# Kernel tuning notes

Measured on AMD Instinct MI355X. Metric: run time of the kernel, lower is better.

The kernel has to match this reference:

```python
import jax, jax.numpy as jnp
import numpy as np
jax.config.update("jax_enable_x64", True)

MAX_DEPTH = 21
SENTINEL = np.int64(2 ** 62)  # pads invalid (consumed) slots; > any real morton code


def split_by3(n):
    n = n & 2097151
    n = (n | (n << 32)) & 8725724278095871
    n = (n | (n << 16)) & 8725728556220671
    n = (n | (n << 8)) & 1157144660301377551
    n = (n | (n << 4)) & 1207822528635744451
    n = (n | (n << 2)) & 1317624576693539401
    return n


def _unique_agg(codes, feats):
    # codes: [N] sorted int64 (SENTINEL-padded at the end); feats: [N, F]
    # Emulates torch.unique_consecutive + scatter_add with fixed shapes.
    N = codes.shape[0]
    is_new = jnp.concatenate([jnp.ones((1,), dtype=bool), codes[1:] != codes[:-1]])
    seg = jnp.cumsum(is_new) - 1  # consecutive-group id (reverse index)
    agg = jax.ops.segment_sum(feats, seg, num_segments=N)
    ucodes = jnp.full((N,), SENTINEL, dtype=jnp.int64).at[seg].set(codes)
    count = jnp.sum(is_new & (codes != SENTINEL)).astype(jnp.int32)
    return ucodes, agg, count


def setup_inputs() -> dict:
    key = jax.random.key(0)
    N = 262144
    new_cloud = jax.random.normal(key, (N, 4), dtype=jnp.float32)
    leaf_size = jnp.full((3,), 0.1, dtype=jnp.float32)
    return {"new_cloud": new_cloud, "leaf_size": leaf_size}


def reference(new_cloud, leaf_size):
    xyz = new_cloud[:, :3]
    n = new_cloud.shape[0]
    # aggregated features: [count=1, xyz, xyz^2, extra cols]
    feats = jnp.concatenate(
        [jnp.ones((n, 1), new_cloud.dtype), xyz, xyz * xyz, new_cloud[:, 3:]], axis=1
    )
    origin = jnp.min(xyz, axis=0) - 0.5 * leaf_size
    ijk = jnp.floor((xyz - origin) / leaf_size).astype(jnp.int64)
    s = split_by3(ijk)
    codes = s[:, 0] | (s[:, 1] << 1) | (s[:, 2] << 2)
    order = jnp.argsort(codes)
    codes = codes[order]
    feats = feats[order]
    mc, ag, cnt = _unique_agg(codes, feats)
    mcs, ags, cnts = [mc], [ag], [cnt]
    for d in range(1, MAX_DEPTH):
        shifted = jnp.where(mc == SENTINEL, SENTINEL, mc >> 3)
        mc, ag, cnt = _unique_agg(shifted, ag)
        mcs.append(mc)
        ags.append(ag)
        cnts.append(cnt)
    # [MAX_DEPTH, N] codes (SENTINEL-padded), [MAX_DEPTH, N, F] aggregates (zero-padded), [MAX_DEPTH] valid counts
    return jnp.stack(mcs), jnp.stack(ags), jnp.stack(cnts)
```

## Files before the change

kernel.cpp:

```cpp
#include <hip/hip_runtime.h>
#include <stdint.h>

static constexpr int L0N = 2097152;
static constexpr int O1 = 0,      S1 = 262144;
static constexpr int O2 = 262144, S2 = 32768;
static constexpr int O3 = 294912, S3 = 4096;
static constexpr int O4 = 299008, S4 = 512;
static constexpr int O5 = 300032, S5 = 64;
static constexpr int O6 = 301056, S6 = 8;
static constexpr int O7 = 302080;
static constexpr int UP_TOT = 303104;
static constexpr int UNBLK = 296;

__device__ __forceinline__ unsigned s3_r9(unsigned n){
  n &= 0x3FFu;
  n = (n | (n << 16)) & 0x030000FFu;
  n = (n | (n << 8))  & 0x0300F00Fu;
  n = (n | (n << 4))  & 0x030C30C3u;
  n = (n | (n << 2))  & 0x09249249u;
  return n;
}

__device__ __forceinline__ void wave_block_min3(float& mx, float& my, float& mz, int tid){
  #pragma unroll
  for (int o = 32; o; o >>= 1){
    mx = fminf(mx, __shfl_down(mx, o, 64));
    my = fminf(my, __shfl_down(my, o, 64));
    mz = fminf(mz, __shfl_down(mz, o, 64));
  }
  __shared__ float sm[3][4];
  int lane = tid & 63, wid = tid >> 6;
  if (lane == 0){ sm[0][wid] = mx; sm[1][wid] = my; sm[2][wid] = mz; }
  __syncthreads();
  if (tid == 0){
    for (int w = 1; w < 4; w++){
      mx = fminf(mx, sm[0][w]); my = fminf(my, sm[1][w]); mz = fminf(mz, sm[2][w]);
    }
  }
}

__global__ void kminzero_r9(const float4* __restrict__ cloud, int n,
                            int* __restrict__ C0, float* __restrict__ pmins){
  int gid = blockIdx.x * blockDim.x + threadIdx.x;
  int gstride = gridDim.x * blockDim.x;
  int4 z = {0,0,0,0};
  for (int v = gid; v < L0N / 4; v += gstride)
    ((int4*)C0)[v] = z;
  float mx = INFINITY, my = INFINITY, mz = INFINITY;
  for (int i = gid; i < n; i += gstride){
    float4 p = cloud[i];
    mx = fminf(mx, p.x); my = fminf(my, p.y); mz = fminf(mz, p.z);
  }
  wave_block_min3(mx, my, mz, threadIdx.x);
  if (threadIdx.x == 0){
    pmins[3 * blockIdx.x + 0] = mx;
    pmins[3 * blockIdx.x + 1] = my;
    pmins[3 * blockIdx.x + 2] = mz;
  }
}

__global__ void kmin2_r9(const float* __restrict__ pmins, float* __restrict__ mins){
  int t = threadIdx.x;
  float mx = pmins[3 * t + 0];
  float my = pmins[3 * t + 1];
  float mz = pmins[3 * t + 2];
  wave_block_min3(mx, my, mz, t);
  if (t == 0){ mins[0] = mx; mins[1] = my; mins[2] = mz; }
}

__global__ void kA_r9(const float4* __restrict__ cloud, const float* __restrict__ leaf,
                      const float* __restrict__ mins, int n,
                      int* __restrict__ C0, int2* __restrict__ CR){
  int i = blockIdx.x * blockDim.x + threadIdx.x;
  if (i >= n) return;
  float lx = leaf[0], ly = leaf[1], lz = leaf[2];
  float ox = mins[0] - 0.5f * lx;
  float oy = mins[1] - 0.5f * ly;
  float oz = mins[2] - 0.5f * lz;
  float4 p = cloud[i];
  int ix = (int)floorf((p.x - ox) / lx);
  int iy = (int)floorf((p.y - oy) / ly);
  int iz = (int)floorf((p.z - oz) / lz);
  ix = min(max(ix, 0), 127); iy = min(max(iy, 0), 127); iz = min(max(iz, 0), 127);
  int code = (int)(s3_r9((unsigned)ix) | (s3_r9((unsigned)iy) << 1) | (s3_r9((unsigned)iz) << 2));
  int rank = atomicAdd(C0 + code, 1);
  CR[i] = {code, rank};
}

__device__ __forceinline__ int block_scan_incl(int v, int tid, int* total){
  __shared__ int w4[4];
  __syncthreads();
  int lane = tid & 63, wid = tid >> 6;
  #pragma unroll
  for (int o = 1; o < 64; o <<= 1){
    int n = __shfl_up(v, o, 64);
    if (lane >= o) v += n;
  }
  if (lane == 63) w4[wid] = v;
  __syncthreads();
  if (tid < 4){
    int w = w4[tid];
    #pragma unroll
    for (int o = 1; o < 4; o <<= 1){
      int n = __shfl_up(w, o, 4);
      if (tid >= o) w += n;
    }
    w4[tid] = w;
  }
  __syncthreads();
  if (wid > 0) v += w4[wid - 1];
  *total = w4[3];
  return v;
}

__global__ void ksA1_r9(const int* __restrict__ C0, int* __restrict__ cntTot,
                        int* __restrict__ flagTot){
  int b = blockIdx.x, t = threadIdx.x;
  const int4* c4 = (const int4*)(C0 + (size_t)b * 2048 + t * 8);
  int4 a = c4[0], d = c4[1];
  int cs = a.x + a.y + a.z + a.w + d.x + d.y + d.z + d.w;
  int fs = (a.x!=0)+(a.y!=0)+(a.z!=0)+(a.w!=0)+(d.x!=0)+(d.y!=0)+(d.z!=0)+(d.w!=0);
  int ctot, ftot;
  block_scan_incl(cs, t, &ctot);
  block_scan_incl(fs, t, &ftot);
  if (t == 0){ cntTot[b] = ctot; flagTot[b] = ftot; }
}

__global__ void ksA2_r9(const int* __restrict__ cntTot, const int* __restrict__ flagTot,
                        int* __restrict__ cntBase, int* __restrict__ flagBase,
                        float* __restrict__ cnts){
  int t = threadIdx.x;
  int ccarry = 0, fcarry = 0;
  for (int c = 0; c < 1024; c += 256){
    int cv = cntTot[c + t], fv = flagTot[c + t];
    int ctot, ftot;
    int ci = block_scan_incl(cv, t, &ctot);
    int fi = block_scan_incl(fv, t, &ftot);
    cntBase[c + t] = ccarry + (ci - cv);
    flagBase[c + t] = fcarry + (fi - fv);
    ccarry += ctot; fcarry += ftot;
  }
  if (t == 0) cnts[0] = (float)fcarry;
}

__global__ void ksA3_r9(const int* __restrict__ C0, const int* __restrict__ cntBase,
                        int* __restrict__ E){
  int b = blockIdx.x, t = threadIdx.x;
  const int4* c4 = (const int4*)(C0 + (size_t)b * 2048 + t * 8);
  int4 a = c4[0], d = c4[1];
  int k[8] = {a.x, a.y, a.z, a.w, d.x, d.y, d.z, d.w};
  int cs = k[0]+k[1]+k[2]+k[3]+k[4]+k[5]+k[6]+k[7];
  int tot;
  int incl = block_scan_incl(cs, t, &tot);
  int e = cntBase[b] + (incl - cs);
  int ev[8];
  #pragma unroll
  for (int c = 0; c < 8; c++){ ev[c] = e; e += k[c]; }
  int4* e4 = (int4*)(E + (size_t)b * 2048 + t * 8);
  e4[0] = {ev[0], ev[1], ev[2], ev[3]};
  e4[1] = {ev[4], ev[5], ev[6], ev[7]};
}

__global__ void kplace_r9(const float4* __restrict__ cloud, const int2* __restrict__ CR,
                          const int* __restrict__ E, int n, float4* __restrict__ S){
  int i = blockIdx.x * blockDim.x + threadIdx.x;
  if (i >= n) return;
  int2 cr = CR[i];
  S[E[cr.x] + cr.y] = cloud[i];
}

__global__ void kbuild1f_r9(const float4* __restrict__ S, const int* __restrict__ C0,
                            const int* __restrict__ E, const int* __restrict__ flagBase,
                            float* __restrict__ PU, int* __restrict__ CU,
                            float* __restrict__ out, int N){
  int p = blockIdx.x * blockDim.x + threadIdx.x;
  int b = blockIdx.x;
  int s0 = 8 * p;
  const int4* c4 = (const int4*)(C0 + s0);
  int4 ca = c4[0], cb = c4[1];
  int k[8] = {ca.x, ca.y, ca.z, ca.w, cb.x, cb.y, cb.z, cb.w};
  const int4* e4 = (const int4*)(E + s0);
  int4 ea = e4[0], eb = e4[1];
  int eo[8] = {ea.x, ea.y, ea.z, ea.w, eb.x, eb.y, eb.z, eb.w};
  float4 recA[8], recB[8];
  float4 pa = {0,0,0,0}, pb = {0,0,0,0};
  int fs = 0;
  #pragma unroll
  for (int c = 0; c < 8; c++){
    if (k[c] > 0){
      float4 a = {0,0,0,0}, bb = {0,0,0,0};
      int base = eo[c];
      for (int j = 0; j < k[c]; j++){
        float4 pt = S[base + j];
        a.x += 1.0f;        a.y += pt.x;        a.z += pt.y;        a.w += pt.z;
        bb.x += pt.x*pt.x;  bb.y += pt.y*pt.y;  bb.z += pt.z*pt.z;  bb.w += pt.w;
      }
      recA[c] = a; recB[c] = bb;
      pa.x += a.x; pa.y += a.y; pa.z += a.z; pa.w += a.w;
      pb.x += bb.x; pb.y += bb.y; pb.z += bb.z; pb.w += bb.w;
      fs++;
    }
  }
  int tot;
  int incl = block_scan_incl(fs, threadIdx.x, &tot);
  int pos = flagBase[b] + (incl - fs);
  size_t MCS = (size_t)21 * N;
  #pragma unroll
  for (int c = 0; c < 8; c++){
    if (k[c] > 0){
      out[pos] = (float)(s0 + c);
      float4* ag = (float4*)(out + MCS + (size_t)pos * 8);
      ag[0] = recA[c]; ag[1] = recB[c];
      pos++;
    }
  }
  float4* prec = (float4*)(PU + (size_t)p * 8);
  prec[0] = pa; prec[1] = pb;
  CU[p] = (int)pa.x;
}

__device__ __forceinline__ void build_one_r9(float* __restrict__ PU, int* __restrict__ CU,
                                             int srcOff, int dstOff, int p){
  const float4* s = (const float4*)(PU + (size_t)(srcOff + 8 * p) * 8);
  float4 a = {0,0,0,0}, b = {0,0,0,0};
  #pragma unroll
  for (int c = 0; c < 8; c++){
    float4 u = s[2 * c], v = s[2 * c + 1];
    a.x += u.x; a.y += u.y; a.z += u.z; a.w += u.w;
    b.x += v.x; b.y += v.y; b.z += v.z; b.w += v.w;
  }
  float4* d = (float4*)(PU + (size_t)(dstOff + p) * 8);
  d[0] = a; d[1] = b;
  CU[dstOff + p] = (int)a.x;
}

__global__ void kbuild_r9(float* __restrict__ PU, int* __restrict__ CU,
                          int srcOff, int dstOff, int ndst){
  int p = blockIdx.x * blockDim.x + threadIdx.x;
  if (p >= ndst) return;
  build_one_r9(PU, CU, srcOff, dstOff, p);
}

__global__ void kbuildtail_r9(float* __restrict__ PU, int* __restrict__ CU){
  for (int i = O4 + S4 + threadIdx.x; i < UP_TOT; i += blockDim.x)
    CU[i] = 0;
  __syncthreads();
  const int so[4]   = {O3, O4, O5, O6};
  const int dofs[4] = {O4, O5, O6, O7};
  const int nd[4]   = {S4, S5, S6, 1};
  for (int l = 0; l < 4; l++){
    for (int p = threadIdx.x; p < nd[l]; p += blockDim.x)
      build_one_r9(PU, CU, so[l], dofs[l], p);
    __syncthreads();
  }
}

__global__ void kscan1_r9(const int* __restrict__ CU, int* __restrict__ partials){
  int b = blockIdx.x, t = threadIdx.x;
  int4 v = ((const int4*)CU)[(size_t)b * 256 + t];
  int c = (v.x != 0) + (v.y != 0) + (v.z != 0) + (v.w != 0);
  int tot;
  block_scan_incl(c, t, &tot);
  if (t == 0) partials[b] = tot;
}

__global__ void kscan2_r9(const int* __restrict__ partials, int* __restrict__ base,
                          float* __restrict__ cnts){
  int t = threadIdx.x;
  __shared__ int s[UNBLK];
  for (int i = t; i < UNBLK; i += 256) s[i] = partials[i];
  __syncthreads();
  const int bb[8] = {0, 256, 288, 292, 293, 294, 295, 296};
  for (int L = 0; L < 7; L++){
    int beg = bb[L], end = bb[L + 1];
    int carry = 0;
    for (int c = beg; c < end; c += 256){
      int idx = c + t;
      int v = (idx < end) ? s[idx] : 0;
      int tot;
      int incl = block_scan_incl(v, t, &tot);
      if (idx < end) base[idx] = carry + (incl - v);
      carry += tot;
    }
    if (t == 0){
      if (L < 6) cnts[L + 1] = (float)carry;
      else { for (int d = 7; d < 21; d++) cnts[d] = (float)carry; }
    }
  }
}

__global__ void kscan3_r9(const float* __restrict__ PU, const int* __restrict__ CU,
                          const int* __restrict__ base, float* __restrict__ out, int N){
  int b = blockIdx.x, t = threadIdx.x;
  int lvl, soff;
  if      (b < 256){ lvl = 1; soff = O1; }
  else if (b < 288){ lvl = 2; soff = O2; }
  else if (b < 292){ lvl = 3; soff = O3; }
  else if (b < 293){ lvl = 4; soff = O4; }
  else if (b < 294){ lvl = 5; soff = O5; }
  else if (b < 295){ lvl = 6; soff = O6; }
  else             { lvl = 7; soff = O7; }
  int slot0 = b * 1024 + t * 4;
  int4 v = ((const int4*)CU)[(size_t)b * 256 + t];
  int fl[4] = { v.x != 0, v.y != 0, v.z != 0, v.w != 0 };
  int c = fl[0] + fl[1] + fl[2] + fl[3];
  int tot;
  int incl = block_scan_incl(c, t, &tot);
  int p = base[b] + (incl - c);
  size_t MCS = (size_t)21 * N;
  #pragma unroll
  for (int kk = 0; kk < 4; kk++){
    if (fl[kk]){
      int slot = slot0 + kk;
      out[(size_t)lvl * N + p] = (float)(slot - soff);
      const float4* rec = (const float4*)(PU + (size_t)slot * 8);
      float4* ag = (float4*)(out + MCS + ((size_t)lvl * N + p) * 8);
      ag[0] = rec[0]; ag[1] = rec[1];
      p++;
    }
  }
}

__global__ void kfinal_r9(const float* __restrict__ PU, float* __restrict__ out, int N){
  size_t MCS = (size_t)21 * N;
  int i = threadIdx.x;
  if (i < 104){
    int d = 8 + (i >> 3), q = i & 7;
    out[MCS + ((size_t)d * N) * 8 + q] = PU[(size_t)O7 * 8 + q];
  } else if (i < 117){
    int d = 8 + (i - 104);
    out[(size_t)d * N] = 0.0f;
  }
}

extern "C" void kernel_launch(void* const* d_in, const int* in_sizes, int n_in,
                              void* d_out, int out_size, void* d_ws, size_t ws_size,
                              hipStream_t stream){
  int ci = 0, li = 1;
  if (n_in >= 2 && in_sizes[0] == 3){ ci = 1; li = 0; }
  const float4* cloud = (const float4*)d_in[ci];
  const float*  leaf  = (const float*)d_in[li];
  int N = in_sizes[ci] / 4;

  float* out = (float*)d_out;
  float* PU   = (float*)d_ws;
  int*   C0   = (int*)(PU + (size_t)UP_TOT * 8);
  int*   CU   = C0 + L0N;
  int*   E    = CU + UP_TOT;
  int2*  CR   = (int2*)(E + L0N);
  float4* S   = (float4*)(CR + N);
  int* cntTot = (int*)(S + N);
  int* flagTot = cntTot + 1024;
  int* cntBase = flagTot + 1024;
  int* flagBase = cntBase + 1024;
  int* partU  = flagBase + 1024;
  int* baseU  = partU + UNBLK;
  float* pmins = (float*)(baseU + UNBLK);
  float* mins  = pmins + 768;
  float* cnts  = out + (size_t)189 * N;

  kminzero_r9<<<256, 256, 0, stream>>>(cloud, N, C0, pmins);
  kmin2_r9<<<1, 256, 0, stream>>>(pmins, mins);

  kA_r9<<<(N + 255) / 256, 256, 0, stream>>>(cloud, leaf, mins, N, C0, CR);
  ksA1_r9<<<1024, 256, 0, stream>>>(C0, cntTot, flagTot);
  ksA2_r9<<<1,    256, 0, stream>>>(cntTot, flagTot, cntBase, flagBase, cnts);
  ksA3_r9<<<1024, 256, 0, stream>>>(C0, cntBase, E);
  kplace_r9<<<(N + 255) / 256, 256, 0, stream>>>(cloud, CR, E, N, S);

  kbuild1f_r9<<<1024, 256, 0, stream>>>(S, C0, E, flagBase, PU, CU, out, N);
  kbuild_r9<<<128, 256, 0, stream>>>(PU, CU, O1, O2, S2);
  kbuild_r9<<<16,  256, 0, stream>>>(PU, CU, O2, O3, S3);
  kbuildtail_r9<<<1, 256, 0, stream>>>(PU, CU);

  kscan1_r9<<<UNBLK, 256, 0, stream>>>(CU, partU);
  kscan2_r9<<<1,     256, 0, stream>>>(partU, baseU, cnts);
  kscan3_r9<<<UNBLK, 256, 0, stream>>>(PU, CU, baseU, out, N);
  kfinal_r9<<<1, 128, 0, stream>>>(PU, out, N);
}
```

Baseline: 304.6 us.

## Fuse pipeline into fewer launches with decoupled look-back scans and grid spin barriers

Reduces the kernel count from fifteen to six. The min-reduction finalize moves into the binning kernel through an atomic flag. The three-pass count/flag scans become single-pass decoupled look-back scans. Place and level-1 build are merged behind a grid-wide spin barrier, as are the upper-level builds. The aim is to remove launch gaps and tiny serial kernels. The cost is that the spin barriers assume all blocks are co-resident: with 1024 blocks and launch bounds of 4 per CU this risks deadlock, and it also adds atomic polling overhead.

```diff
diff --git a/kernel.cpp b/kernel.cpp
--- a/kernel.cpp
+++ b/kernel.cpp
@@ -2,7 +2,7 @@
 #include <stdint.h>
 
 static constexpr int L0N = 2097152;
-static constexpr int O1 = 0,      S1 = 262144;
+static constexpr int O1 = 0;
 static constexpr int O2 = 262144, S2 = 32768;
 static constexpr int O3 = 294912, S3 = 4096;
 static constexpr int O4 = 299008, S4 = 512;
@@ -12,7 +12,7 @@
 static constexpr int UP_TOT = 303104;
 static constexpr int UNBLK = 296;
 
-__device__ __forceinline__ unsigned s3_r9(unsigned n){
+__device__ __forceinline__ unsigned s3_rA(unsigned n){
   n &= 0x3FFu;
   n = (n | (n << 16)) & 0x030000FFu;
   n = (n | (n << 8))  & 0x0300F00Fu;
@@ -21,70 +21,8 @@
   return n;
 }
 
-__device__ __forceinline__ void wave_block_min3(float& mx, float& my, float& mz, int tid){
-  #pragma unroll
-  for (int o = 32; o; o >>= 1){
-    mx = fminf(mx, __shfl_down(mx, o, 64));
-    my = fminf(my, __shfl_down(my, o, 64));
-    mz = fminf(mz, __shfl_down(mz, o, 64));
-  }
-  __shared__ float sm[3][4];
-  int lane = tid & 63, wid = tid >> 6;
-  if (lane == 0){ sm[0][wid] = mx; sm[1][wid] = my; sm[2][wid] = mz; }
-  __syncthreads();
-  if (tid == 0){
-    for (int w = 1; w < 4; w++){
-      mx = fminf(mx, sm[0][w]); my = fminf(my, sm[1][w]); mz = fminf(mz, sm[2][w]);
-    }
-  }
-}
-
-__global__ void kminzero_r9(const float4* __restrict__ cloud, int n,
-                            int* __restrict__ C0, float* __restrict__ pmins){
-  int gid = blockIdx.x * blockDim.x + threadIdx.x;
-  int gstride = gridDim.x * blockDim.x;
-  int4 z = {0,0,0,0};
-  for (int v = gid; v < L0N / 4; v += gstride)
-    ((int4*)C0)[v] = z;
-  float mx = INFINITY, my = INFINITY, mz = INFINITY;
-  for (int i = gid; i < n; i += gstride){
-    float4 p = cloud[i];
-    mx = fminf(mx, p.x); my = fminf(my, p.y); mz = fminf(mz, p.z);
-  }
-  wave_block_min3(mx, my, mz, threadIdx.x);
-  if (threadIdx.x == 0){
-    pmins[3 * blockIdx.x + 0] = mx;
-    pmins[3 * blockIdx.x + 1] = my;
-    pmins[3 * blockIdx.x + 2] = mz;
-  }
-}
-
-__global__ void kmin2_r9(const float* __restrict__ pmins, float* __restrict__ mins){
-  int t = threadIdx.x;
-  float mx = pmins[3 * t + 0];
-  float my = pmins[3 * t + 1];
-  float mz = pmins[3 * t + 2];
-  wave_block_min3(mx, my, mz, t);
-  if (t == 0){ mins[0] = mx; mins[1] = my; mins[2] = mz; }
-}
-
-__global__ void kA_r9(const float4* __restrict__ cloud, const float* __restrict__ leaf,
-                      const float* __restrict__ mins, int n,
-                      int* __restrict__ C0, int2* __restrict__ CR){
-  int i = blockIdx.x * blockDim.x + threadIdx.x;
-  if (i >= n) return;
-  float lx = leaf[0], ly = leaf[1], lz = leaf[2];
-  float ox = mins[0] - 0.5f * lx;
-  float oy = mins[1] - 0.5f * ly;
-  float oz = mins[2] - 0.5f * lz;
-  float4 p = cloud[i];
-  int ix = (int)floorf((p.x - ox) / lx);
-  int iy = (int)floorf((p.y - oy) / ly);
-  int iz = (int)floorf((p.z - oz) / lz);
-  ix = min(max(ix, 0), 127); iy = min(max(iy, 0), 127); iz = min(max(iz, 0), 127);
-  int code = (int)(s3_r9((unsigned)ix) | (s3_r9((unsigned)iy) << 1) | (s3_r9((unsigned)iz) << 2));
-  int rank = atomicAdd(C0 + code, 1);
-  CR[i] = {code, rank};
+__device__ __forceinline__ unsigned long long packE(unsigned st, unsigned c, unsigned f){
+  return ((unsigned long long)st << 62) | ((unsigned long long)c << 21) | (unsigned long long)f;
 }
 
 __device__ __forceinline__ int block_scan_incl(int v, int tid, int* total){
@@ -113,46 +51,157 @@
   return v;
 }
 
-__global__ void ksA1_r9(const int* __restrict__ C0, int* __restrict__ cntTot,
-                        int* __restrict__ flagTot){
-  int b = blockIdx.x, t = threadIdx.x;
-  const int4* c4 = (const int4*)(C0 + (size_t)b * 2048 + t * 8);
-  int4 a = c4[0], d = c4[1];
-  int cs = a.x + a.y + a.z + a.w + d.x + d.y + d.z + d.w;
-  int fs = (a.x!=0)+(a.y!=0)+(a.z!=0)+(a.w!=0)+(d.x!=0)+(d.y!=0)+(d.z!=0)+(d.w!=0);
-  int ctot, ftot;
-  block_scan_incl(cs, t, &ctot);
-  block_scan_incl(fs, t, &ftot);
-  if (t == 0){ cntTot[b] = ctot; flagTot[b] = ftot; }
-}
-
-__global__ void ksA2_r9(const int* __restrict__ cntTot, const int* __restrict__ flagTot,
-                        int* __restrict__ cntBase, int* __restrict__ flagBase,
-                        float* __restrict__ cnts){
+__device__ __forceinline__ void grid_spin_barrier(int* ctr, int nblocks){
+  __threadfence();
+  __syncthreads();
+  if (threadIdx.x == 0){
+    atomicAdd(ctr, 1);
+    while (atomicAdd(ctr, 0) < nblocks) ;
+  }
+  __syncthreads();
+  __threadfence();
+}
+
+__device__ __forceinline__ void wave_block_min3(float& mx, float& my, float& mz, int tid){
+  #pragma unroll
+  for (int o = 32; o; o >>= 1){
+    mx = fminf(mx, __shfl_down(mx, o, 64));
+    my = fminf(my, __shfl_down(my, o, 64));
+    mz = fminf(mz, __shfl_down(mz, o, 64));
+  }
+  __shared__ float sm[3][4];
+  int lane = tid & 63, wid = tid >> 6;
+  if (lane == 0){ sm[0][wid] = mx; sm[1][wid] = my; sm[2][wid] = mz; }
+  __syncthreads();
+  if (tid == 0){
+    for (int w = 1; w < 4; w++){
+      mx = fminf(mx, sm[0][w]); my = fminf(my, sm[1][w]); mz = fminf(mz, sm[2][w]);
+    }
+  }
+}
+
+__global__ void kminzero_rA(const float4* __restrict__ cloud, int n,
+                            int* __restrict__ C0, int* __restrict__ aux, int auxN,
+                            float* __restrict__ pmins){
+  int gid = blockIdx.x * blockDim.x + threadIdx.x;
+  int gstride = gridDim.x * blockDim.x;
+  int4 z = {0,0,0,0};
+  for (int v = gid; v < L0N / 4; v += gstride)
+    ((int4*)C0)[v] = z;
+  if (gid < auxN) aux[gid] = 0;
+  float mx = INFINITY, my = INFINITY, mz = INFINITY;
+  for (int i = gid; i < n; i += gstride){
+    float4 p = cloud[i];
+    mx = fminf(mx, p.x); my = fminf(my, p.y); mz = fminf(mz, p.z);
+  }
+  wave_block_min3(mx, my, mz, threadIdx.x);
+  if (threadIdx.x == 0){
+    pmins[3 * blockIdx.x + 0] = mx;
+    pmins[3 * blockIdx.x + 1] = my;
+    pmins[3 * blockIdx.x + 2] = mz;
+  }
+}
+
+__global__ __launch_bounds__(256, 4)
+void kA_rA(const float4* __restrict__ cloud, const float* __restrict__ leaf,
+           const float* __restrict__ pmins, unsigned* __restrict__ mA, int n,
+           int* __restrict__ C0, int2* __restrict__ CR){
   int t = threadIdx.x;
-  int ccarry = 0, fcarry = 0;
-  for (int c = 0; c < 1024; c += 256){
-    int cv = cntTot[c + t], fv = flagTot[c + t];
-    int ctot, ftot;
-    int ci = block_scan_incl(cv, t, &ctot);
-    int fi = block_scan_incl(fv, t, &ftot);
-    cntBase[c + t] = ccarry + (ci - cv);
-    flagBase[c + t] = fcarry + (fi - fv);
-    ccarry += ctot; fcarry += ftot;
-  }
-  if (t == 0) cnts[0] = (float)fcarry;
-}
-
-__global__ void ksA3_r9(const int* __restrict__ C0, const int* __restrict__ cntBase,
-                        int* __restrict__ E){
+  if (blockIdx.x == 0){
+    float mx = pmins[3 * t + 0];
+    float my = pmins[3 * t + 1];
+    float mz = pmins[3 * t + 2];
+    wave_block_min3(mx, my, mz, t);
+    if (t == 0){
+      atomicExch(&mA[0], __float_as_uint(mx));
+      atomicExch(&mA[1], __float_as_uint(my));
+      atomicExch(&mA[2], __float_as_uint(mz));
+      __threadfence();
+      atomicExch(&mA[3], 1u);
+    }
+  }
+  __shared__ float sox, soy, soz, slx, sly, slz;
+  if (t == 0){
+    while (atomicAdd(&mA[3], 0u) == 0u) ;
+    __threadfence();
+    float lx = leaf[0], ly = leaf[1], lz = leaf[2];
+    slx = lx; sly = ly; slz = lz;
+    sox = __uint_as_float(atomicAdd(&mA[0], 0u)) - 0.5f * lx;
+    soy = __uint_as_float(atomicAdd(&mA[1], 0u)) - 0.5f * ly;
+    soz = __uint_as_float(atomicAdd(&mA[2], 0u)) - 0.5f * lz;
+  }
+  __syncthreads();
+  int i = blockIdx.x * 256 + t;
+  if (i >= n) return;
+  float4 p = cloud[i];
+  int ix = (int)floorf((p.x - sox) / slx);
+  int iy = (int)floorf((p.y - soy) / sly);
+  int iz = (int)floorf((p.z - soz) / slz);
+  ix = min(max(ix, 0), 127); iy = min(max(iy, 0), 127); iz = min(max(iz, 0), 127);
+  int code = (int)(s3_rA((unsigned)ix) | (s3_rA((unsigned)iy) << 1) | (s3_rA((unsigned)iz) << 2));
+  int rank = atomicAdd(C0 + code, 1);
+  CR[i] = {code, rank};
+}
+
+__global__ __launch_bounds__(256, 4)
+void kscanE_rA(const int* __restrict__ C0, int* __restrict__ E,
+               int* __restrict__ flagBase, unsigned long long* __restrict__ statusE,
+               float* __restrict__ cnts){
   int b = blockIdx.x, t = threadIdx.x;
   const int4* c4 = (const int4*)(C0 + (size_t)b * 2048 + t * 8);
   int4 a = c4[0], d = c4[1];
   int k[8] = {a.x, a.y, a.z, a.w, d.x, d.y, d.z, d.w};
-  int cs = k[0]+k[1]+k[2]+k[3]+k[4]+k[5]+k[6]+k[7];
-  int tot;
-  int incl = block_scan_incl(cs, t, &tot);
-  int e = cntBase[b] + (incl - cs);
+  int cs = 0, fs = 0;
+  #pragma unroll
+  for (int c = 0; c < 8; c++){ cs += k[c]; fs += (k[c] != 0); }
+  int cTot, fTot;
+  int ic = block_scan_incl(cs, t, &cTot);
+  int dummyTot;
+  block_scan_incl(fs, t, &dummyTot);
+  fTot = dummyTot;
+  if (t == 0)
+    atomicExch(&statusE[b], packE(b == 0 ? 2u : 1u, (unsigned)cTot, (unsigned)fTot));
+  __shared__ unsigned eCs, eFs;
+  if (b == 0){
+    if (t == 0){ eCs = 0; eFs = 0; }
+  } else if (t < 64){
+    unsigned sum_c = 0, sum_f = 0;
+    int offset = 0;
+    bool done = false;
+    while (!done){
+      int idx = b - 1 - offset - t;
+      unsigned long long v = 0;
+      unsigned st = 2;
+      if (idx >= 0){
+        do { v = atomicAdd(&statusE[idx], 0ULL); st = (unsigned)(v >> 62); } while (st == 0);
+      }
+      unsigned long long m2 = __ballot(st == 2);
+      if (m2){
+        int f2 = __ffsll((unsigned long long)m2) - 1;
+        if (t <= f2){ sum_c += (unsigned)((v >> 21) & 0x1FFFFFu); sum_f += (unsigned)(v & 0x1FFFFFu); }
+        done = true;
+      } else {
+        sum_c += (unsigned)((v >> 21) & 0x1FFFFFu); sum_f += (unsigned)(v & 0x1FFFFFu);
+        offset += 64;
+      }
+    }
+    #pragma unroll
+    for (int o = 32; o; o >>= 1){
+      sum_c += __shfl_down(sum_c, o, 64);
+      sum_f += __shfl_down(sum_f, o, 64);
+    }
+    if (t == 0){
+      eCs = sum_c; eFs = sum_f;
+      atomicExch(&statusE[b], packE(2u, sum_c + (unsigned)cTot, sum_f + (unsigned)fTot));
+    }
+  }
+  __syncthreads();
+  unsigned eC = eCs, eF = eFs;
+  if (t == 0){
+    flagBase[b] = (int)eF;
+    if (b == 1023) cnts[0] = (float)(eF + (unsigned)fTot);
+  }
+  int e = (int)eC + (ic - cs);
   int ev[8];
   #pragma unroll
   for (int c = 0; c < 8; c++){ ev[c] = e; e += k[c]; }
@@ -161,30 +210,34 @@
   e4[1] = {ev[4], ev[5], ev[6], ev[7]};
 }
 
-__global__ void kplace_r9(const float4* __restrict__ cloud, const int2* __restrict__ CR,
-                          const int* __restrict__ E, int n, float4* __restrict__ S){
-  int i = blockIdx.x * blockDim.x + threadIdx.x;
-  if (i >= n) return;
-  int2 cr = CR[i];
-  S[E[cr.x] + cr.y] = cloud[i];
-}
-
-__global__ void kbuild1f_r9(const float4* __restrict__ S, const int* __restrict__ C0,
-                            const int* __restrict__ E, const int* __restrict__ flagBase,
-                            float* __restrict__ PU, int* __restrict__ CU,
-                            float* __restrict__ out, int N){
-  int p = blockIdx.x * blockDim.x + threadIdx.x;
-  int b = blockIdx.x;
-  int s0 = 8 * p;
+__global__ __launch_bounds__(256, 4)
+void kplacebuild_rA(const float4* __restrict__ cloud, const int2* __restrict__ CR,
+                    const int* __restrict__ C0, const int* __restrict__ E,
+                    const int* __restrict__ flagBase, int n, float4* __restrict__ S,
+                    float* __restrict__ PU, int* __restrict__ CU,
+                    float* __restrict__ out, int N, int* __restrict__ ctr){
+  int b = blockIdx.x, t = threadIdx.x;
+  int i = b * 256 + t;
+  if (i < n){
+    int2 cr = CR[i];
+    S[E[cr.x] + cr.y] = cloud[i];
+  }
+  grid_spin_barrier(ctr, gridDim.x);
+  int s0 = 8 * i;
   const int4* c4 = (const int4*)(C0 + s0);
   int4 ca = c4[0], cb = c4[1];
   int k[8] = {ca.x, ca.y, ca.z, ca.w, cb.x, cb.y, cb.z, cb.w};
   const int4* e4 = (const int4*)(E + s0);
   int4 ea = e4[0], eb = e4[1];
   int eo[8] = {ea.x, ea.y, ea.z, ea.w, eb.x, eb.y, eb.z, eb.w};
-  float4 recA[8], recB[8];
+  int fs = 0;
+  #pragma unroll
+  for (int c = 0; c < 8; c++) fs += (k[c] != 0);
+  int tot;
+  int incl = block_scan_incl(fs, t, &tot);
+  int pos = flagBase[b] + (incl - fs);
+  size_t MCS = (size_t)21 * N;
   float4 pa = {0,0,0,0}, pb = {0,0,0,0};
-  int fs = 0;
   #pragma unroll
   for (int c = 0; c < 8; c++){
     if (k[c] > 0){
@@ -195,31 +248,20 @@
         a.x += 1.0f;        a.y += pt.x;        a.z += pt.y;        a.w += pt.z;
         bb.x += pt.x*pt.x;  bb.y += pt.y*pt.y;  bb.z += pt.z*pt.z;  bb.w += pt.w;
       }
-      recA[c] = a; recB[c] = bb;
+      out[pos] = (float)(s0 + c);
+      float4* ag = (float4*)(out + MCS + (size_t)pos * 8);
+      ag[0] = a; ag[1] = bb;
+      pos++;
       pa.x += a.x; pa.y += a.y; pa.z += a.z; pa.w += a.w;
       pb.x += bb.x; pb.y += bb.y; pb.z += bb.z; pb.w += bb.w;
-      fs++;
-    }
-  }
-  int tot;
-  int incl = block_scan_incl(fs, threadIdx.x, &tot);
-  int pos = flagBase[b] + (incl - fs);
-  size_t MCS = (size_t)21 * N;
-  #pragma unroll
-  for (int c = 0; c < 8; c++){
-    if (k[c] > 0){
-      out[pos] = (float)(s0 + c);
-      float4* ag = (float4*)(out + MCS + (size_t)pos * 8);
-      ag[0] = recA[c]; ag[1] = recB[c];
-      pos++;
-    }
-  }
-  float4* prec = (float4*)(PU + (size_t)p * 8);
+    }
+  }
+  float4* prec = (float4*)(PU + (size_t)i * 8);
   prec[0] = pa; prec[1] = pb;
-  CU[p] = (int)pa.x;
-}
-
-__device__ __forceinline__ void build_one_r9(float* __restrict__ PU, int* __restrict__ CU,
+  CU[i] = (int)pa.x;
+}
+
+__device__ __forceinline__ void build_one_rA(float* __restrict__ PU, int* __restrict__ CU,
                                              int srcOff, int dstOff, int p){
   const float4* s = (const float4*)(PU + (size_t)(srcOff + 8 * p) * 8);
   float4 a = {0,0,0,0}, b = {0,0,0,0};
@@ -234,80 +276,96 @@
   CU[dstOff + p] = (int)a.x;
 }
 
-__global__ void kbuild_r9(float* __restrict__ PU, int* __restrict__ CU,
-                          int srcOff, int dstOff, int ndst){
-  int p = blockIdx.x * blockDim.x + threadIdx.x;
-  if (p >= ndst) return;
-  build_one_r9(PU, CU, srcOff, dstOff, p);
-}
-
-__global__ void kbuildtail_r9(float* __restrict__ PU, int* __restrict__ CU){
-  for (int i = O4 + S4 + threadIdx.x; i < UP_TOT; i += blockDim.x)
-    CU[i] = 0;
-  __syncthreads();
-  const int so[4]   = {O3, O4, O5, O6};
-  const int dofs[4] = {O4, O5, O6, O7};
-  const int nd[4]   = {S4, S5, S6, 1};
-  for (int l = 0; l < 4; l++){
-    for (int p = threadIdx.x; p < nd[l]; p += blockDim.x)
-      build_one_r9(PU, CU, so[l], dofs[l], p);
-    __syncthreads();
-  }
-}
-
-__global__ void kscan1_r9(const int* __restrict__ CU, int* __restrict__ partials){
+__global__ __launch_bounds__(256, 4)
+void kbuildUp_rA(float* __restrict__ PU, int* __restrict__ CU, int* __restrict__ ctrs){
   int b = blockIdx.x, t = threadIdx.x;
-  int4 v = ((const int4*)CU)[(size_t)b * 256 + t];
-  int c = (v.x != 0) + (v.y != 0) + (v.z != 0) + (v.w != 0);
-  int tot;
-  block_scan_incl(c, t, &tot);
-  if (t == 0) partials[b] = tot;
-}
-
-__global__ void kscan2_r9(const int* __restrict__ partials, int* __restrict__ base,
-                          float* __restrict__ cnts){
-  int t = threadIdx.x;
-  __shared__ int s[UNBLK];
-  for (int i = t; i < UNBLK; i += 256) s[i] = partials[i];
-  __syncthreads();
-  const int bb[8] = {0, 256, 288, 292, 293, 294, 295, 296};
-  for (int L = 0; L < 7; L++){
-    int beg = bb[L], end = bb[L + 1];
-    int carry = 0;
-    for (int c = beg; c < end; c += 256){
-      int idx = c + t;
-      int v = (idx < end) ? s[idx] : 0;
-      int tot;
-      int incl = block_scan_incl(v, t, &tot);
-      if (idx < end) base[idx] = carry + (incl - v);
-      carry += tot;
-    }
-    if (t == 0){
-      if (L < 6) cnts[L + 1] = (float)carry;
-      else { for (int d = 7; d < 21; d++) cnts[d] = (float)carry; }
-    }
-  }
-}
-
-__global__ void kscan3_r9(const float* __restrict__ PU, const int* __restrict__ CU,
-                          const int* __restrict__ base, float* __restrict__ out, int N){
+  build_one_rA(PU, CU, O1, O2, b * 256 + t);
+  grid_spin_barrier(&ctrs[0], 128);
+  if (t < 32) build_one_rA(PU, CU, O2, O3, b * 32 + t);
+  grid_spin_barrier(&ctrs[1], 128);
+  if (b != 0) return;
+  for (int i2 = O4 + S4 + t; i2 < UP_TOT; i2 += 256) CU[i2] = 0;
+  __syncthreads();
+  for (int p = t; p < S4; p += 256) build_one_rA(PU, CU, O3, O4, p);
+  __syncthreads();
+  if (t < S5) build_one_rA(PU, CU, O4, O5, t);
+  __syncthreads();
+  if (t < S6) build_one_rA(PU, CU, O5, O6, t);
+  __syncthreads();
+  if (t == 0) build_one_rA(PU, CU, O6, O7, 0);
+}
+
+__global__ __launch_bounds__(256, 4)
+void kscanU_rA(const float* __restrict__ PU, const int* __restrict__ CU,
+               unsigned long long* __restrict__ statusU,
+               float* __restrict__ out, float* __restrict__ cnts, int N){
   int b = blockIdx.x, t = threadIdx.x;
-  int lvl, soff;
-  if      (b < 256){ lvl = 1; soff = O1; }
-  else if (b < 288){ lvl = 2; soff = O2; }
-  else if (b < 292){ lvl = 3; soff = O3; }
-  else if (b < 293){ lvl = 4; soff = O4; }
-  else if (b < 294){ lvl = 5; soff = O5; }
-  else if (b < 295){ lvl = 6; soff = O6; }
-  else             { lvl = 7; soff = O7; }
+  size_t MCS = (size_t)21 * N;
+  if (b == UNBLK){
+    if (t < 104){
+      int dd = 8 + (t >> 3), q = t & 7;
+      out[MCS + ((size_t)dd * N) * 8 + q] = PU[(size_t)O7 * 8 + q];
+    } else if (t < 117){
+      int dd = 8 + (t - 104);
+      out[(size_t)dd * N] = 0.0f;
+    }
+    return;
+  }
+  int lvl, soff, segStart, lastTile;
+  if      (b < 256){ lvl = 1; soff = O1; segStart = 0;   lastTile = 255; }
+  else if (b < 288){ lvl = 2; soff = O2; segStart = 256; lastTile = 287; }
+  else if (b < 292){ lvl = 3; soff = O3; segStart = 288; lastTile = 291; }
+  else if (b < 293){ lvl = 4; soff = O4; segStart = 292; lastTile = 292; }
+  else if (b < 294){ lvl = 5; soff = O5; segStart = 293; lastTile = 293; }
+  else if (b < 295){ lvl = 6; soff = O6; segStart = 294; lastTile = 294; }
+  else             { lvl = 7; soff = O7; segStart = 295; lastTile = 295; }
   int slot0 = b * 1024 + t * 4;
   int4 v = ((const int4*)CU)[(size_t)b * 256 + t];
   int fl[4] = { v.x != 0, v.y != 0, v.z != 0, v.w != 0 };
   int c = fl[0] + fl[1] + fl[2] + fl[3];
   int tot;
   int incl = block_scan_incl(c, t, &tot);
-  int p = base[b] + (incl - c);
-  size_t MCS = (size_t)21 * N;
+  if (t == 0)
+    atomicExch(&statusU[b], ((unsigned long long)(b == segStart ? 2u : 1u) << 62)
+                            | (unsigned long long)(unsigned)tot);
+  __shared__ unsigned eFs;
+  if (b == segStart){
+    if (t == 0) eFs = 0;
+  } else if (t < 64){
+    unsigned sum_f = 0;
+    int offset = 0;
+    bool done = false;
+    while (!done){
+      int idx = b - 1 - offset - t;
+      unsigned long long vv = 0;
+      unsigned st = 2;
+      if (idx >= segStart){
+        do { vv = atomicAdd(&statusU[idx], 0ULL); st = (unsigned)(vv >> 62); } while (st == 0);
+      }
+      unsigned long long m2 = __ballot(st == 2);
+      if (m2){
+        int f2 = __ffsll((unsigned long long)m2) - 1;
+        if (t <= f2) sum_f += (unsigned)(vv & 0x3FFFFFFFu);
+        done = true;
+      } else {
+        sum_f += (unsigned)(vv & 0x3FFFFFFFu);
+        offset += 64;
+      }
+    }
+    #pragma unroll
+    for (int o = 32; o; o >>= 1) sum_f += __shfl_down(sum_f, o, 64);
+    if (t == 0){
+      eFs = sum_f;
+      atomicExch(&statusU[b], (2ULL << 62) | (unsigned long long)(sum_f + (unsigned)tot));
+    }
+  }
+  __syncthreads();
+  int p = (int)eFs + (incl - c);
+  if (t == 0 && b == lastTile){
+    float total = (float)(eFs + (unsigned)tot);
+    if (lvl < 7) cnts[lvl] = total;
+    else { for (int dd = 7; dd < 21; dd++) cnts[dd] = total; }
+  }
   #pragma unroll
   for (int kk = 0; kk < 4; kk++){
     if (fl[kk]){
@@ -321,18 +379,6 @@
   }
 }
 
-__global__ void kfinal_r9(const float* __restrict__ PU, float* __restrict__ out, int N){
-  size_t MCS = (size_t)21 * N;
-  int i = threadIdx.x;
-  if (i < 104){
-    int d = 8 + (i >> 3), q = i & 7;
-    out[MCS + ((size_t)d * N) * 8 + q] = PU[(size_t)O7 * 8 + q];
-  } else if (i < 117){
-    int d = 8 + (i - 104);
-    out[(size_t)d * N] = 0.0f;
-  }
-}
-
 extern "C" void kernel_launch(void* const* d_in, const int* in_sizes, int n_in,
                               void* d_out, int out_size, void* d_ws, size_t ws_size,
                               hipStream_t stream){
@@ -349,32 +395,21 @@
   int*   E    = CU + UP_TOT;
   int2*  CR   = (int2*)(E + L0N);
   float4* S   = (float4*)(CR + N);
-  int* cntTot = (int*)(S + N);
-  int* flagTot = cntTot + 1024;
-  int* cntBase = flagTot + 1024;
-  int* flagBase = cntBase + 1024;
-  int* partU  = flagBase + 1024;
-  int* baseU  = partU + UNBLK;
-  float* pmins = (float*)(baseU + UNBLK);
-  float* mins  = pmins + 768;
-  float* cnts  = out + (size_t)189 * N;
-
-  kminzero_r9<<<256, 256, 0, stream>>>(cloud, N, C0, pmins);
-  kmin2_r9<<<1, 256, 0, stream>>>(pmins, mins);
-
-  kA_r9<<<(N + 255) / 256, 256, 0, stream>>>(cloud, leaf, mins, N, C0, CR);
-  ksA1_r9<<<1024, 256, 0, stream>>>(C0, cntTot, flagTot);
-  ksA2_r9<<<1,    256, 0, stream>>>(cntTot, flagTot, cntBase, flagBase, cnts);
-  ksA3_r9<<<1024, 256, 0, stream>>>(C0, cntBase, E);
-  kplace_r9<<<(N + 255) / 256, 256, 0, stream>>>(cloud, CR, E, N, S);
-
-  kbuild1f_r9<<<1024, 256, 0, stream>>>(S, C0, E, flagBase, PU, CU, out, N);
-  kbuild_r9<<<128, 256, 0, stream>>>(PU, CU, O1, O2, S2);
-  kbuild_r9<<<16,  256, 0, stream>>>(PU, CU, O2, O3, S3);
-  kbuildtail_r9<<<1, 256, 0, stream>>>(PU, CU);
-
-  kscan1_r9<<<UNBLK, 256, 0, stream>>>(CU, partU);
-  kscan2_r9<<<1,     256, 0, stream>>>(partU, baseU, cnts);
-  kscan3_r9<<<UNBLK, 256, 0, stream>>>(PU, CU, baseU, out, N);
-  kfinal_r9<<<1, 128, 0, stream>>>(PU, out, N);
-}
+  unsigned long long* statusE = (unsigned long long*)(S + N);
+  unsigned long long* statusU = statusE + 1024;
+  int* flagBase = (int*)(statusU + 512);
+  int* ctrs     = flagBase + 1024;
+  unsigned* mA  = (unsigned*)(ctrs + 4);
+  float* pmins  = (float*)(mA + 4);
+  int* auxZero  = (int*)statusE;
+  int auxN      = 2048 + 1024 + 1024 + 4 + 4;
+  float* cnts   = out + (size_t)189 * N;
+
+  kminzero_rA<<<256, 256, 0, stream>>>(cloud, N, C0, auxZero, auxN, pmins);
+  kA_rA<<<(N + 255) / 256, 256, 0, stream>>>(cloud, leaf, pmins, mA, N, C0, CR);
+  kscanE_rA<<<1024, 256, 0, stream>>>(C0, E, flagBase, statusE, cnts);
+  kplacebuild_rA<<<(N + 255) / 256, 256, 0, stream>>>(cloud, CR, C0, E, flagBase,
+                                                      N, S, PU, CU, out, N, &ctrs[0]);
+  kbuildUp_rA<<<128, 256, 0, stream>>>(PU, CU, &ctrs[1]);
+  kscanU_rA<<<UNBLK + 1, 256, 0, stream>>>(PU, CU, statusU, out, cnts, N);
+}
```

Result: slower. 622.5 us (+104.3%).
